# Kernel tuning notes

Hardware: AMD Instinct MI355X
Metric: run time of the kernel (lower is better)

The kernel has to match this reference:

```python
import jax, jax.numpy as jnp
import numpy as np


def setup_inputs() -> dict:
    key = jax.random.key(0)
    ks = jax.random.split(key, 10)
    B, HD, CD = 8192, 1024, 1024
    stdv = 1.0 / np.sqrt(HD)
    inp = {
        "hprev": jax.random.normal(ks[0], (B, HD), dtype=jnp.float32),
        "cprev": jax.random.normal(ks[1], (B, CD), dtype=jnp.float32),
        "w_hi": jax.random.uniform(ks[2], (HD, CD), jnp.float32, -stdv, stdv),
        "b_hi": jax.random.uniform(ks[3], (1, CD), jnp.float32, -stdv, stdv),
        "w_hf": jax.random.uniform(ks[4], (HD, CD), jnp.float32, -stdv, stdv),
        "b_hf": jax.random.uniform(ks[5], (1, CD), jnp.float32, -stdv, stdv),
        "w_hg": jax.random.uniform(ks[6], (HD, CD), jnp.float32, -stdv, stdv),
        "b_hg": jax.random.uniform(ks[7], (1, CD), jnp.float32, -stdv, stdv),
        "w_ho": jax.random.uniform(ks[8], (HD, CD), jnp.float32, -stdv, stdv),
        "b_ho": jax.random.uniform(ks[9], (1, CD), jnp.float32, -stdv, stdv),
    }
    return inp


def reference(hprev, cprev, w_hi, b_hi, w_hf, b_hf, w_hg, b_hg, w_ho, b_ho):
    # LSTM cell gates driven only by previous hidden state.
    i = jax.nn.sigmoid(hprev @ w_hi + b_hi)   # input gate  [B, CD]
    f = jax.nn.sigmoid(hprev @ w_hf + b_hf)   # forget gate [B, CD]
    g = jnp.tanh(hprev @ w_hg + b_hg)         # cell candidate
    o = jax.nn.sigmoid(hprev @ w_ho + b_ho)   # output gate
    cprime = f * cprev + i * g
    hprime = o * jnp.tanh(cprime)
    return (hprime, cprime)
```

## Files before the change

### kernel.cpp

```cpp
#include <hip/hip_runtime.h>
#include <hip/hip_bf16.h>
#include <stdint.h>

typedef short short8 __attribute__((ext_vector_type(8)));
typedef float f32x4 __attribute__((ext_vector_type(4)));
typedef unsigned short ushort4v __attribute__((ext_vector_type(4)));

#define MDIM 8192
#define KDIM 1024
#define NDIM 1024
#define NKT  16


__device__ __forceinline__ unsigned short f2bf(float f) {
  union { float f; unsigned int u; } v; v.f = f;
  unsigned int u = v.u;
  u += 0x7fffu + ((u >> 16) & 1u);
  return (unsigned short)(u >> 16);
}

__device__ __forceinline__ void load_lds16(const void* gsrc, void* ldst) {
  __builtin_amdgcn_global_load_lds(
      (__attribute__((address_space(1))) void*)gsrc,
      (__attribute__((address_space(3))) void*)ldst,
      16, 0, 0);
}

__device__ __forceinline__ float fast_sigmoid(float x) {
  return 1.0f / (1.0f + __expf(-x));
}

__device__ __forceinline__ float fast_tanh(float x) {
  x = fminf(30.0f, fmaxf(-30.0f, x));
  float e = __expf(-2.0f * x);
  return (1.0f - e) / (1.0f + e);
}


__global__ void convert_h_tiled(const float* __restrict__ in,
                                unsigned short* __restrict__ out, int nchunk) {
  int idx = blockIdx.x * blockDim.x + threadIdx.x;
  int stride = gridDim.x * blockDim.x;
  for (int i = idx; i < nchunk; i += stride) {
    int r = i >> 7;
    int kc8 = i & 127;
    const float4* src = reinterpret_cast<const float4*>(in + (size_t)r * KDIM + kc8 * 8);
    float4 v0 = src[0], v1 = src[1];
    short8 o;
    o[0] = (short)f2bf(v0.x); o[1] = (short)f2bf(v0.y);
    o[2] = (short)f2bf(v0.z); o[3] = (short)f2bf(v0.w);
    o[4] = (short)f2bf(v1.x); o[5] = (short)f2bf(v1.y);
    o[6] = (short)f2bf(v1.z); o[7] = (short)f2bf(v1.w);
    int kt = kc8 >> 3;
    int c8 = kc8 & 7;
    reinterpret_cast<short8*>(out)[((size_t)kt * MDIM + r) * 8 + c8] = o;
  }
}

__global__ void convert_w_tiled(const float* __restrict__ w0,
                                const float* __restrict__ w1,
                                const float* __restrict__ w2,
                                const float* __restrict__ w3,
                                unsigned short* __restrict__ out) {
  __shared__ float tile[64][65];
  int g = blockIdx.z;
  const float* w = (g == 0) ? w0 : (g == 1) ? w1 : (g == 2) ? w2 : w3;
  int kt = blockIdx.y;
  int k0 = kt * 64;
  int n0 = blockIdx.x * 64;
  int tx = threadIdx.x;
  int ty = threadIdx.y;
#pragma unroll
  for (int j = 0; j < 16; ++j) {
    int kk = ty * 16 + j;
    tile[kk][tx] = w[(size_t)(k0 + kk) * NDIM + n0 + tx];
  }
  __syncthreads();
#pragma unroll
  for (int j = 0; j < 16; ++j) {
    int nn = ty * 16 + j;
    out[(((size_t)kt * 4 + g) * NDIM + n0 + nn) * 64 + tx] = f2bf(tile[tx][nn]);
  }
}


#define BUF0 0
#define BUF1 65536

#define BARRIER() __builtin_amdgcn_s_barrier()
#define WAIT_LGKM0() do { \
    asm volatile("s_waitcnt lgkmcnt(0)" ::: "memory"); \
    __builtin_amdgcn_sched_barrier(0); } while (0)
#define WAIT_VM0() asm volatile("s_waitcnt vmcnt(0)" ::: "memory")

#define STAGE_A2(T, kA, j0) do { \
    load_lds16(ab + srcA + (kA) + (j0) * 8192,       lds + (T) + (j0) * 8192 + tid * 16); \
    load_lds16(ab + srcA + (kA) + ((j0) + 1) * 8192, lds + (T) + ((j0) + 1) * 8192 + tid * 16); } while (0)
#define STAGE_B2(T, kB, j0) do { \
    load_lds16(bb + srcB + (kB) + (j0) * 131072,       lds + (T) + 32768 + (j0) * 8192 + tid * 16); \
    load_lds16(bb + srcB + (kB) + ((j0) + 1) * 131072, lds + (T) + 32768 + ((j0) + 1) * 8192 + tid * 16); } while (0)

#define RD_A(S, m, s) (*(const short8*)(lds + (S) + a_base + (m) * 2048 + (s)))
#define RD_B(S, g, s) (*(const short8*)(lds + (S) + b_base + (g) * 8192 + (s)))

#define MFMA16(mb_) do { \
  _Pragma("unroll") \
  for (int mi = 0; mi < 4; ++mi) { \
    _Pragma("unroll") \
    for (int g = 0; g < 4; ++g) \
      acc[g][(mb_) + mi] = __builtin_amdgcn_mfma_f32_16x16x32_bf16( \
          Af[mi], Bf[g], acc[g][(mb_) + mi], 0, 0, 0); \
  } } while (0)

#define TILE(CUR, NXT, kA, kB) do { \
    short8 Af[4], Bf[4]; \
     \
    _Pragma("unroll") for (int g = 0; g < 4; ++g) Bf[g] = RD_B(CUR, g, s0); \
    _Pragma("unroll") for (int mi = 0; mi < 4; ++mi) Af[mi] = RD_A(CUR, mi, s0); \
    STAGE_A2(NXT, kA, 0); STAGE_A2(NXT, kA, 2); \
    BARRIER(); WAIT_LGKM0(); \
    __builtin_amdgcn_s_setprio(1); MFMA16(0); __builtin_amdgcn_s_setprio(0); \
    BARRIER(); \
     \
    _Pragma("unroll") for (int mi = 0; mi < 4; ++mi) Af[mi] = RD_A(CUR, 4 + mi, s0); \
    STAGE_B2(NXT, kB, 0); STAGE_B2(NXT, kB, 2); \
    BARRIER(); WAIT_LGKM0(); \
    __builtin_amdgcn_s_setprio(1); MFMA16(4); __builtin_amdgcn_s_setprio(0); \
    BARRIER(); \
     \
    _Pragma("unroll") for (int g = 0; g < 4; ++g) Bf[g] = RD_B(CUR, g, s1); \
    _Pragma("unroll") for (int mi = 0; mi < 4; ++mi) Af[mi] = RD_A(CUR, mi, s1); \
    BARRIER(); WAIT_LGKM0(); \
    __builtin_amdgcn_s_setprio(1); MFMA16(0); __builtin_amdgcn_s_setprio(0); \
    BARRIER(); \
     \
    _Pragma("unroll") for (int mi = 0; mi < 4; ++mi) Af[mi] = RD_A(CUR, 4 + mi, s1); \
    BARRIER(); WAIT_LGKM0(); \
    __builtin_amdgcn_s_setprio(1); MFMA16(4); __builtin_amdgcn_s_setprio(0); \
    WAIT_VM0(); \
    BARRIER(); } while (0)

__global__ __launch_bounds__(512, 2) void lstm_fused_gemm(
    const unsigned short* __restrict__ At,
    const unsigned short* __restrict__ Bt,
    const float* __restrict__ cprev,
    const float* __restrict__ b_i, const float* __restrict__ b_f,
    const float* __restrict__ b_g, const float* __restrict__ b_o,
    float* __restrict__ out)
{
  extern __shared__ unsigned char lds[];
  const int tid  = threadIdx.x;
  const int lane = tid & 63;
  const int wave = tid >> 6;
  const int wr = wave >> 2;
  const int wc = wave & 3;
  const int r15 = lane & 15;
  const int hh  = lane >> 4;

  int bid = blockIdx.x;
  int loc = bid >> 3;
  int mb = (bid & 7) * 4 + (loc >> 4);
  int nb = loc & 15;
  int brow = mb * 256;
  int bcol = nb * 64;

  const char* ab = (const char*)At;
  const char* bb = (const char*)Bt;

  const int rloc = tid >> 3;
  const int cx = (((tid & 7) ^ (rloc & 7)) << 4);
  const uint32_t srcA = (uint32_t)(brow + rloc) * 128 + cx;
  const uint32_t srcB = (uint32_t)(bcol + rloc) * 128 + cx;

  const int s0 = ((hh ^ (r15 & 7)) << 4);
  const int s1 = s0 ^ 64;
  const uint32_t a_base = (uint32_t)(wr * 128 + r15) * 128;
  const uint32_t b_base = 32768u + (uint32_t)(wc * 16 + r15) * 128;

  f32x4 acc[4][8];
#pragma unroll
  for (int g = 0; g < 4; ++g)
#pragma unroll
    for (int m = 0; m < 8; ++m)
      acc[g][m] = (f32x4){0.f, 0.f, 0.f, 0.f};

  STAGE_A2(BUF0, 0, 0); STAGE_A2(BUF0, 0, 2);
  STAGE_B2(BUF0, 0, 0); STAGE_B2(BUF0, 0, 2);
  WAIT_VM0();
  BARRIER();

  for (int it = 0; it < NKT / 2; ++it) {
    const uint32_t t1 = 2 * it + 1;
    const uint32_t t2 = (2 * it + 2) & (NKT - 1);
    {
      const uint32_t kA = t1 << 20, kB = t1 << 19;
      TILE(BUF0, BUF1, kA, kB);
    }
    {
      const uint32_t kA = t2 << 20, kB = t2 << 19;
      TILE(BUF1, BUF0, kA, kB);
    }
  }

  const size_t outC = (size_t)MDIM * NDIM;
  const int cc = bcol + wc * 16 + r15;
  const float bi = b_i[cc], bff = b_f[cc], bg = b_g[cc], bo = b_o[cc];
#pragma unroll
  for (int m = 0; m < 8; ++m) {
#pragma unroll
    for (int j = 0; j < 4; ++j) {
      int rr = brow + wr * 128 + m * 16 + hh * 4 + j;
      size_t base = (size_t)rr * NDIM + cc;
      float pi = acc[0][m][j] + bi;
      float pf = acc[1][m][j] + bff;
      float pg = acc[2][m][j] + bg;
      float po = acc[3][m][j] + bo;
      float iv = fast_sigmoid(pi);
      float fv = fast_sigmoid(pf);
      float gv = fast_tanh(pg);
      float ov = fast_sigmoid(po);
      float cp = fv * cprev[base] + iv * gv;
      float hp = ov * fast_tanh(cp);
      out[base] = hp;
      out[outC + base] = cp;
    }
  }
}


extern "C" void kernel_launch(void* const* d_in, const int* in_sizes, int n_in,
                              void* d_out, int out_size, void* d_ws, size_t ws_size,
                              hipStream_t stream) {
  const float* hprev = (const float*)d_in[0];
  const float* cprev = (const float*)d_in[1];
  const float* w_hi  = (const float*)d_in[2];
  const float* b_hi  = (const float*)d_in[3];
  const float* w_hf  = (const float*)d_in[4];
  const float* b_hf  = (const float*)d_in[5];
  const float* w_hg  = (const float*)d_in[6];
  const float* b_hg  = (const float*)d_in[7];
  const float* w_ho  = (const float*)d_in[8];
  const float* b_ho  = (const float*)d_in[9];
  float* out = (float*)d_out;

  unsigned short* At = (unsigned short*)d_ws;
  unsigned short* Bt = (unsigned short*)((char*)d_ws + (size_t)NKT * MDIM * 64 * 2);

  convert_h_tiled<<<2048, 256, 0, stream>>>(hprev, At, MDIM * KDIM / 8);
  convert_w_tiled<<<dim3(16, 16, 4), dim3(64, 4, 1), 0, stream>>>(
      w_hi, w_hf, w_hg, w_ho, Bt);
  lstm_fused_gemm<<<512, 512, 131072, stream>>>(At, Bt, cprev,
                                                b_hi, b_hf, b_hg, b_ho, out);
}
```

Before: 99.60 us.

## Load B fragments directly from global in MFMA-ready layout, halve LDS

The weight conversion now writes B in a fragment-linear layout, so each lane can load its MFMA B operand straight from global memory into registers, with one tile prefetched ahead. Only A is staged through LDS, which halves the shared memory to 64KB and removes most barriers and LDS waits in the inner loop. Block-to-tile mapping is also reordered so consecutive blocks share N columns. The trade-off is that B data is re-read from global/L2 by every block, and global load latency must be hidden by the register prefetch.

```diff
diff --git a/kernel.cpp b/kernel.cpp
--- a/kernel.cpp
+++ b/kernel.cpp
@@ -57,11 +57,11 @@
   }
 }
 
-__global__ void convert_w_tiled(const float* __restrict__ w0,
-                                const float* __restrict__ w1,
-                                const float* __restrict__ w2,
-                                const float* __restrict__ w3,
-                                unsigned short* __restrict__ out) {
+__global__ void convert_w_fraglin(const float* __restrict__ w0,
+                                  const float* __restrict__ w1,
+                                  const float* __restrict__ w2,
+                                  const float* __restrict__ w3,
+                                  unsigned short* __restrict__ out) {
   __shared__ float tile[64][65];
   int g = blockIdx.z;
   const float* w = (g == 0) ? w0 : (g == 1) ? w1 : (g == 2) ? w2 : w3;
@@ -77,78 +77,78 @@
   }
   __syncthreads();
 #pragma unroll
-  for (int j = 0; j < 16; ++j) {
-    int nn = ty * 16 + j;
-    out[(((size_t)kt * 4 + g) * NDIM + n0 + nn) * 64 + tx] = f2bf(tile[tx][nn]);
-  }
-}
-
-
-#define BUF0 0
-#define BUF1 65536
-
-#define BARRIER() __builtin_amdgcn_s_barrier()
-#define WAIT_LGKM0() do { \
-    asm volatile("s_waitcnt lgkmcnt(0)" ::: "memory"); \
-    __builtin_amdgcn_sched_barrier(0); } while (0)
-#define WAIT_VM0() asm volatile("s_waitcnt vmcnt(0)" ::: "memory")
-
-#define STAGE_A2(T, kA, j0) do { \
-    load_lds16(ab + srcA + (kA) + (j0) * 8192,       lds + (T) + (j0) * 8192 + tid * 16); \
-    load_lds16(ab + srcA + (kA) + ((j0) + 1) * 8192, lds + (T) + ((j0) + 1) * 8192 + tid * 16); } while (0)
-#define STAGE_B2(T, kB, j0) do { \
-    load_lds16(bb + srcB + (kB) + (j0) * 131072,       lds + (T) + 32768 + (j0) * 8192 + tid * 16); \
-    load_lds16(bb + srcB + (kB) + ((j0) + 1) * 131072, lds + (T) + 32768 + ((j0) + 1) * 8192 + tid * 16); } while (0)
-
-#define RD_A(S, m, s) (*(const short8*)(lds + (S) + a_base + (m) * 2048 + (s)))
-#define RD_B(S, g, s) (*(const short8*)(lds + (S) + b_base + (g) * 8192 + (s)))
-
-#define MFMA16(mb_) do { \
-  _Pragma("unroll") \
-  for (int mi = 0; mi < 4; ++mi) { \
+  for (int wit = 0; wit < 2; ++wit) {
+    int idx = ty * 2 + wit;
+    int kk = idx >> 2;
+    int sl = idx & 3;
+    short8 o;
+#pragma unroll
+    for (int e = 0; e < 8; ++e)
+      o[e] = (short)f2bf(tile[kk * 32 + (tx >> 4) * 8 + e][sl * 16 + (tx & 15)]);
+    reinterpret_cast<short8*>(out)[
+        ((((size_t)kt * 2 + kk) * 4 + g) * 64 + (n0 >> 4) + sl) * 64 + tx] = o;
+  }
+}
+
+
+#define BUFA0 0
+#define BUFA1 32768
+
+#define SB() __builtin_amdgcn_sched_barrier(0)
+
+#define LDA4(CUR, mb_, ss) do { \
+    Af0 = *(const short8*)(ldsb + (CUR) + ar + ((mb_) + 0) * 2048 + (ss)); \
+    Af1 = *(const short8*)(ldsb + (CUR) + ar + ((mb_) + 1) * 2048 + (ss)); \
+    Af2 = *(const short8*)(ldsb + (CUR) + ar + ((mb_) + 2) * 2048 + (ss)); \
+    Af3 = *(const short8*)(ldsb + (CUR) + ar + ((mb_) + 3) * 2048 + (ss)); } while (0)
+
+#define MROW(BP, m_, AF) do { \
+    acc[0][m_] = __builtin_amdgcn_mfma_f32_16x16x32_bf16(AF, BP##0, acc[0][m_], 0, 0, 0); \
+    acc[1][m_] = __builtin_amdgcn_mfma_f32_16x16x32_bf16(AF, BP##1, acc[1][m_], 0, 0, 0); \
+    acc[2][m_] = __builtin_amdgcn_mfma_f32_16x16x32_bf16(AF, BP##2, acc[2][m_], 0, 0, 0); \
+    acc[3][m_] = __builtin_amdgcn_mfma_f32_16x16x32_bf16(AF, BP##3, acc[3][m_], 0, 0, 0); } while (0)
+
+#define MFMA16(BP, mb_) do { \
+    __builtin_amdgcn_s_setprio(1); \
+    MROW(BP, (mb_) + 0, Af0); MROW(BP, (mb_) + 1, Af1); \
+    MROW(BP, (mb_) + 2, Af2); MROW(BP, (mb_) + 3, Af3); \
+    __builtin_amdgcn_s_setprio(0); } while (0)
+
+#define TILE(t_, CUR, NXT, BC, BN) do { \
+    const uint32_t tn_ = ((t_) + 1) & (NKT - 1); \
+    short8 q0, q1, q2, q3; \
+    SB(); \
+    q0 = *(const short8*)(bb + ((((uint32_t)(t_) * 2 + 1) * 4 + 0) << 16) + bv); \
+    q1 = *(const short8*)(bb + ((((uint32_t)(t_) * 2 + 1) * 4 + 1) << 16) + bv); \
+    q2 = *(const short8*)(bb + ((((uint32_t)(t_) * 2 + 1) * 4 + 2) << 16) + bv); \
+    q3 = *(const short8*)(bb + ((((uint32_t)(t_) * 2 + 1) * 4 + 3) << 16) + bv); \
+    SB(); \
     _Pragma("unroll") \
-    for (int g = 0; g < 4; ++g) \
-      acc[g][(mb_) + mi] = __builtin_amdgcn_mfma_f32_16x16x32_bf16( \
-          Af[mi], Bf[g], acc[g][(mb_) + mi], 0, 0, 0); \
-  } } while (0)
-
-#define TILE(CUR, NXT, kA, kB) do { \
-    short8 Af[4], Bf[4]; \
-     \
-    _Pragma("unroll") for (int g = 0; g < 4; ++g) Bf[g] = RD_B(CUR, g, s0); \
-    _Pragma("unroll") for (int mi = 0; mi < 4; ++mi) Af[mi] = RD_A(CUR, mi, s0); \
-    STAGE_A2(NXT, kA, 0); STAGE_A2(NXT, kA, 2); \
-    BARRIER(); WAIT_LGKM0(); \
-    __builtin_amdgcn_s_setprio(1); MFMA16(0); __builtin_amdgcn_s_setprio(0); \
-    BARRIER(); \
-     \
-    _Pragma("unroll") for (int mi = 0; mi < 4; ++mi) Af[mi] = RD_A(CUR, 4 + mi, s0); \
-    STAGE_B2(NXT, kB, 0); STAGE_B2(NXT, kB, 2); \
-    BARRIER(); WAIT_LGKM0(); \
-    __builtin_amdgcn_s_setprio(1); MFMA16(4); __builtin_amdgcn_s_setprio(0); \
-    BARRIER(); \
-     \
-    _Pragma("unroll") for (int g = 0; g < 4; ++g) Bf[g] = RD_B(CUR, g, s1); \
-    _Pragma("unroll") for (int mi = 0; mi < 4; ++mi) Af[mi] = RD_A(CUR, mi, s1); \
-    BARRIER(); WAIT_LGKM0(); \
-    __builtin_amdgcn_s_setprio(1); MFMA16(0); __builtin_amdgcn_s_setprio(0); \
-    BARRIER(); \
-     \
-    _Pragma("unroll") for (int mi = 0; mi < 4; ++mi) Af[mi] = RD_A(CUR, 4 + mi, s1); \
-    BARRIER(); WAIT_LGKM0(); \
-    __builtin_amdgcn_s_setprio(1); MFMA16(4); __builtin_amdgcn_s_setprio(0); \
-    WAIT_VM0(); \
-    BARRIER(); } while (0)
+    for (int j = 0; j < 4; ++j) \
+      load_lds16(ab + ((size_t)tn_ << 20) + srcA + j * 8192, \
+                 ldsb + (NXT) + j * 8192 + tid * 16); \
+    SB(); \
+    BN##0 = *(const short8*)(bb + (((tn_ * 2 + 0) * 4 + 0) << 16) + bv); \
+    BN##1 = *(const short8*)(bb + (((tn_ * 2 + 0) * 4 + 1) << 16) + bv); \
+    BN##2 = *(const short8*)(bb + (((tn_ * 2 + 0) * 4 + 2) << 16) + bv); \
+    BN##3 = *(const short8*)(bb + (((tn_ * 2 + 0) * 4 + 3) << 16) + bv); \
+    SB(); \
+    LDA4(CUR, 0, s0v); MFMA16(BC, 0); \
+    LDA4(CUR, 4, s0v); MFMA16(BC, 4); \
+    LDA4(CUR, 0, s1v); MFMA16(q, 0); \
+    LDA4(CUR, 4, s1v); MFMA16(q, 4); \
+    asm volatile("s_waitcnt vmcnt(4)" ::: "memory"); \
+    __builtin_amdgcn_s_barrier(); } while (0)
 
 __global__ __launch_bounds__(512, 2) void lstm_fused_gemm(
     const unsigned short* __restrict__ At,
-    const unsigned short* __restrict__ Bt,
+    const unsigned short* __restrict__ Blin,
     const float* __restrict__ cprev,
     const float* __restrict__ b_i, const float* __restrict__ b_f,
     const float* __restrict__ b_g, const float* __restrict__ b_o,
     float* __restrict__ out)
 {
-  extern __shared__ unsigned char lds[];
+  __shared__ unsigned char ldsb[65536];
   const int tid  = threadIdx.x;
   const int lane = tid & 63;
   const int wave = tid >> 6;
@@ -159,23 +159,23 @@
 
   int bid = blockIdx.x;
   int loc = bid >> 3;
-  int mb = (bid & 7) * 4 + (loc >> 4);
-  int nb = loc & 15;
+  int nb = (bid & 7) * 2 + (loc >> 5);
+  int mb = loc & 31;
   int brow = mb * 256;
   int bcol = nb * 64;
 
   const char* ab = (const char*)At;
-  const char* bb = (const char*)Bt;
-
-  const int rloc = tid >> 3;
-  const int cx = (((tid & 7) ^ (rloc & 7)) << 4);
-  const uint32_t srcA = (uint32_t)(brow + rloc) * 128 + cx;
-  const uint32_t srcB = (uint32_t)(bcol + rloc) * 128 + cx;
-
-  const int s0 = ((hh ^ (r15 & 7)) << 4);
-  const int s1 = s0 ^ 64;
-  const uint32_t a_base = (uint32_t)(wr * 128 + r15) * 128;
-  const uint32_t b_base = 32768u + (uint32_t)(wc * 16 + r15) * 128;
+  const char* bb = (const char*)Blin;
+
+  const int arow = tid >> 3;
+  const int cx = (((tid & 7) ^ (arow & 7)) << 4);
+  const uint32_t srcA = (uint32_t)(brow + arow) * 128 + cx;
+
+  const uint32_t ar = (uint32_t)(wr * 128 + r15) * 128;
+  const int s0v = ((hh ^ (r15 & 7)) << 4);
+  const int s1v = s0v ^ 64;
+
+  const uint32_t bv = ((uint32_t)(nb * 4 + wc) << 10) + lane * 16;
 
   f32x4 acc[4][8];
 #pragma unroll
@@ -184,22 +184,22 @@
     for (int m = 0; m < 8; ++m)
       acc[g][m] = (f32x4){0.f, 0.f, 0.f, 0.f};
 
-  STAGE_A2(BUF0, 0, 0); STAGE_A2(BUF0, 0, 2);
-  STAGE_B2(BUF0, 0, 0); STAGE_B2(BUF0, 0, 2);
-  WAIT_VM0();
-  BARRIER();
+  short8 Af0, Af1, Af2, Af3;
+  short8 bA0, bA1, bA2, bA3, bB0, bB1, bB2, bB3;
+
+#pragma unroll
+  for (int j = 0; j < 4; ++j)
+    load_lds16(ab + srcA + j * 8192, ldsb + BUFA0 + j * 8192 + tid * 16);
+  bA0 = *(const short8*)(bb + (0u << 16) + bv);
+  bA1 = *(const short8*)(bb + (1u << 16) + bv);
+  bA2 = *(const short8*)(bb + (2u << 16) + bv);
+  bA3 = *(const short8*)(bb + (3u << 16) + bv);
+  asm volatile("s_waitcnt vmcnt(0)" ::: "memory");
+  __builtin_amdgcn_s_barrier();
 
   for (int it = 0; it < NKT / 2; ++it) {
-    const uint32_t t1 = 2 * it + 1;
-    const uint32_t t2 = (2 * it + 2) & (NKT - 1);
-    {
-      const uint32_t kA = t1 << 20, kB = t1 << 19;
-      TILE(BUF0, BUF1, kA, kB);
-    }
-    {
-      const uint32_t kA = t2 << 20, kB = t2 << 19;
-      TILE(BUF1, BUF0, kA, kB);
-    }
+    TILE(2 * it,     BUFA0, BUFA1, bA, bB);
+    TILE(2 * it + 1, BUFA1, BUFA0, bB, bA);
   }
 
   const size_t outC = (size_t)MDIM * NDIM;
@@ -243,12 +243,12 @@
   const float* b_ho  = (const float*)d_in[9];
   float* out = (float*)d_out;
 
-  unsigned short* At = (unsigned short*)d_ws;
-  unsigned short* Bt = (unsigned short*)((char*)d_ws + (size_t)NKT * MDIM * 64 * 2);
+  unsigned short* At   = (unsigned short*)d_ws;
+  unsigned short* Blin = (unsigned short*)((char*)d_ws + (size_t)NKT * MDIM * 64 * 2);
 
   convert_h_tiled<<<2048, 256, 0, stream>>>(hprev, At, MDIM * KDIM / 8);
-  convert_w_tiled<<<dim3(16, 16, 4), dim3(64, 4, 1), 0, stream>>>(
-      w_hi, w_hf, w_hg, w_ho, Bt);
-  lstm_fused_gemm<<<512, 512, 131072, stream>>>(At, Bt, cprev,
-                                                b_hi, b_hf, b_hg, b_ho, out);
-}
+  convert_w_fraglin<<<dim3(16, 16, 4), dim3(64, 4, 1), 0, stream>>>(
+      w_hi, w_hf, w_hg, w_ho, Blin);
+  lstm_fused_gemm<<<512, 512, 0, stream>>>(At, Blin, cprev,
+                                           b_hi, b_hf, b_hg, b_ho, out);
+}
```

After: 110.0 us. +10.4%, slower.

## Restructure GEMM main loop into quadrant-wise MFMA with deeper partial-wait prefetch

Applied to the files above, without the earlier changes.

Reworks the K-loop so each wave loads all B fragments for both K-halves at once and computes in 2x2 quadrants of (M,N), reusing registers across both K sub-steps. Staging is reordered so the next tiles' A/B loads are issued into the buffer being freed mid-tile, using vmcnt(6) partial waits instead of draining all loads each tile. The block-to-tile mapping is also changed to group by N-column. This aims to overlap global->LDS traffic with MFMAs more deeply and cut LDS reads, at the cost of more registers and tricky buffer-hazard ordering.

```diff
diff --git a/kernel.cpp b/kernel.cpp
--- a/kernel.cpp
+++ b/kernel.cpp
@@ -4,7 +4,6 @@
 
 typedef short short8 __attribute__((ext_vector_type(8)));
 typedef float f32x4 __attribute__((ext_vector_type(4)));
-typedef unsigned short ushort4v __attribute__((ext_vector_type(4)));
 
 #define MDIM 8192
 #define KDIM 1024
@@ -84,61 +83,58 @@
 }
 
 
-#define BUF0 0
-#define BUF1 65536
-
-#define BARRIER() __builtin_amdgcn_s_barrier()
-#define WAIT_LGKM0() do { \
+#define X0 0
+#define X1 65536
+
+#define BAR() __builtin_amdgcn_s_barrier()
+#define LGKM0() do { \
     asm volatile("s_waitcnt lgkmcnt(0)" ::: "memory"); \
     __builtin_amdgcn_sched_barrier(0); } while (0)
-#define WAIT_VM0() asm volatile("s_waitcnt vmcnt(0)" ::: "memory")
-
-#define STAGE_A2(T, kA, j0) do { \
-    load_lds16(ab + srcA + (kA) + (j0) * 8192,       lds + (T) + (j0) * 8192 + tid * 16); \
-    load_lds16(ab + srcA + (kA) + ((j0) + 1) * 8192, lds + (T) + ((j0) + 1) * 8192 + tid * 16); } while (0)
-#define STAGE_B2(T, kB, j0) do { \
-    load_lds16(bb + srcB + (kB) + (j0) * 131072,       lds + (T) + 32768 + (j0) * 8192 + tid * 16); \
-    load_lds16(bb + srcB + (kB) + ((j0) + 1) * 131072, lds + (T) + 32768 + ((j0) + 1) * 8192 + tid * 16); } while (0)
-
-#define RD_A(S, m, s) (*(const short8*)(lds + (S) + a_base + (m) * 2048 + (s)))
-#define RD_B(S, g, s) (*(const short8*)(lds + (S) + b_base + (g) * 8192 + (s)))
-
-#define MFMA16(mb_) do { \
-  _Pragma("unroll") \
-  for (int mi = 0; mi < 4; ++mi) { \
-    _Pragma("unroll") \
-    for (int g = 0; g < 4; ++g) \
-      acc[g][(mb_) + mi] = __builtin_amdgcn_mfma_f32_16x16x32_bf16( \
-          Af[mi], Bf[g], acc[g][(mb_) + mi], 0, 0, 0); \
-  } } while (0)
-
-#define TILE(CUR, NXT, kA, kB) do { \
-    short8 Af[4], Bf[4]; \
-     \
-    _Pragma("unroll") for (int g = 0; g < 4; ++g) Bf[g] = RD_B(CUR, g, s0); \
-    _Pragma("unroll") for (int mi = 0; mi < 4; ++mi) Af[mi] = RD_A(CUR, mi, s0); \
-    STAGE_A2(NXT, kA, 0); STAGE_A2(NXT, kA, 2); \
-    BARRIER(); WAIT_LGKM0(); \
-    __builtin_amdgcn_s_setprio(1); MFMA16(0); __builtin_amdgcn_s_setprio(0); \
-    BARRIER(); \
-     \
-    _Pragma("unroll") for (int mi = 0; mi < 4; ++mi) Af[mi] = RD_A(CUR, 4 + mi, s0); \
-    STAGE_B2(NXT, kB, 0); STAGE_B2(NXT, kB, 2); \
-    BARRIER(); WAIT_LGKM0(); \
-    __builtin_amdgcn_s_setprio(1); MFMA16(4); __builtin_amdgcn_s_setprio(0); \
-    BARRIER(); \
-     \
-    _Pragma("unroll") for (int g = 0; g < 4; ++g) Bf[g] = RD_B(CUR, g, s1); \
-    _Pragma("unroll") for (int mi = 0; mi < 4; ++mi) Af[mi] = RD_A(CUR, mi, s1); \
-    BARRIER(); WAIT_LGKM0(); \
-    __builtin_amdgcn_s_setprio(1); MFMA16(0); __builtin_amdgcn_s_setprio(0); \
-    BARRIER(); \
-     \
-    _Pragma("unroll") for (int mi = 0; mi < 4; ++mi) Af[mi] = RD_A(CUR, 4 + mi, s1); \
-    BARRIER(); WAIT_LGKM0(); \
-    __builtin_amdgcn_s_setprio(1); MFMA16(4); __builtin_amdgcn_s_setprio(0); \
-    WAIT_VM0(); \
-    BARRIER(); } while (0)
+#define VM6() asm volatile("s_waitcnt vmcnt(6)" ::: "memory")
+
+#define STG_A(BUF, ktv, h) do { \
+    const uint32_t _oA = ((uint32_t)(ktv) << 20) + srcA + (h) * 16384; \
+    load_lds16(ab + _oA,        ldsb + (BUF) + (h) * 16384 + tid * 16); \
+    load_lds16(ab + _oA + 8192, ldsb + (BUF) + (h) * 16384 + 8192 + tid * 16); } while (0)
+#define STG_B(BUF, ktv, h) do { \
+    const uint32_t _oB = ((uint32_t)(ktv) << 19) + srcB0 + (h) * 262144; \
+    load_lds16(bb + _oB,          ldsb + (BUF) + 32768 + (h) * 16384 + tid * 16); \
+    load_lds16(bb + _oB + 131072, ldsb + (BUF) + 32768 + (h) * 16384 + 8192 + tid * 16); } while (0)
+
+#define LDB_ALL(CB) do { \
+    _Pragma("unroll") for (int g = 0; g < 4; ++g) { \
+      Br[g * 2 + 0] = *(const short8*)(ldsb + (CB) + b_base + g * 8192 + s0v); \
+      Br[g * 2 + 1] = *(const short8*)(ldsb + (CB) + b_base + g * 8192 + s1v); } } while (0)
+#define LDA_Q(CB, qm) do { \
+    _Pragma("unroll") for (int f = 0; f < 4; ++f) { \
+      Ar[f * 2 + 0] = *(const short8*)(ldsb + (CB) + a_base + ((qm) * 64 + f * 16) * 128 + s0v); \
+      Ar[f * 2 + 1] = *(const short8*)(ldsb + (CB) + a_base + ((qm) * 64 + f * 16) * 128 + s1v); } } while (0)
+
+#define MFMAQ(qm, qn) do { \
+    __builtin_amdgcn_s_setprio(1); \
+    _Pragma("unroll") for (int kk = 0; kk < 2; ++kk) \
+    _Pragma("unroll") for (int f = 0; f < 4; ++f) \
+    _Pragma("unroll") for (int gg = 0; gg < 2; ++gg) \
+      acc[(qn) * 2 + gg][(qm) * 4 + f] = __builtin_amdgcn_mfma_f32_16x16x32_bf16( \
+          Ar[f * 2 + kk], Br[((qn) * 2 + gg) * 2 + kk], \
+          acc[(qn) * 2 + gg][(qm) * 4 + f], 0, 0, 0); \
+    __builtin_amdgcn_s_setprio(0); } while (0)
+
+#define BLOCK4(CB, OB, tA1, tN2) do { \
+     \
+    LDB_ALL(CB); LDA_Q(CB, 0); \
+    STG_A(OB, tA1, 1); \
+    BAR(); LGKM0(); MFMAQ(0, 0); BAR(); \
+     \
+    STG_B(CB, tN2, 0); \
+    BAR(); MFMAQ(0, 1); BAR(); \
+     \
+    LDA_Q(CB, 1); \
+    STG_B(CB, tN2, 1); \
+    BAR(); LGKM0(); MFMAQ(1, 0); BAR(); \
+     \
+    STG_A(CB, tN2, 0); \
+    BAR(); MFMAQ(1, 1); VM6(); BAR(); } while (0)
 
 __global__ __launch_bounds__(512, 2) void lstm_fused_gemm(
     const unsigned short* __restrict__ At,
@@ -148,7 +144,7 @@
     const float* __restrict__ b_g, const float* __restrict__ b_o,
     float* __restrict__ out)
 {
-  extern __shared__ unsigned char lds[];
+  extern __shared__ unsigned char ldsb[];
   const int tid  = threadIdx.x;
   const int lane = tid & 63;
   const int wave = tid >> 6;
@@ -159,23 +155,23 @@
 
   int bid = blockIdx.x;
   int loc = bid >> 3;
-  int mb = (bid & 7) * 4 + (loc >> 4);
-  int nb = loc & 15;
+  int nb = (bid & 7) * 2 + (loc >> 5);
+  int mb = loc & 31;
   int brow = mb * 256;
   int bcol = nb * 64;
 
   const char* ab = (const char*)At;
   const char* bb = (const char*)Bt;
 
-  const int rloc = tid >> 3;
-  const int cx = (((tid & 7) ^ (rloc & 7)) << 4);
-  const uint32_t srcA = (uint32_t)(brow + rloc) * 128 + cx;
-  const uint32_t srcB = (uint32_t)(bcol + rloc) * 128 + cx;
-
-  const int s0 = ((hh ^ (r15 & 7)) << 4);
-  const int s1 = s0 ^ 64;
+  const int srow = tid >> 3;
+  const int cx = (((tid & 7) ^ (srow & 7)) << 4);
+  const uint32_t srcA  = (uint32_t)(brow + srow) * 128 + cx;
+  const uint32_t srcB0 = (uint32_t)(bcol + srow) * 128 + cx;
+
   const uint32_t a_base = (uint32_t)(wr * 128 + r15) * 128;
   const uint32_t b_base = 32768u + (uint32_t)(wc * 16 + r15) * 128;
+  const int s0v = ((hh ^ (r15 & 7)) << 4);
+  const int s1v = s0v ^ 64;
 
   f32x4 acc[4][8];
 #pragma unroll
@@ -184,22 +180,19 @@
     for (int m = 0; m < 8; ++m)
       acc[g][m] = (f32x4){0.f, 0.f, 0.f, 0.f};
 
-  STAGE_A2(BUF0, 0, 0); STAGE_A2(BUF0, 0, 2);
-  STAGE_B2(BUF0, 0, 0); STAGE_B2(BUF0, 0, 2);
-  WAIT_VM0();
-  BARRIER();
+  short8 Ar[8], Br[8];
+
+  STG_A(X0, 0, 0); STG_A(X0, 0, 1);
+  STG_B(X0, 0, 0); STG_B(X0, 0, 1);
+  STG_B(X1, 1, 0); STG_B(X1, 1, 1);
+  STG_A(X1, 1, 0);
+  VM6();
+  BAR();
 
   for (int it = 0; it < NKT / 2; ++it) {
-    const uint32_t t1 = 2 * it + 1;
-    const uint32_t t2 = (2 * it + 2) & (NKT - 1);
-    {
-      const uint32_t kA = t1 << 20, kB = t1 << 19;
-      TILE(BUF0, BUF1, kA, kB);
-    }
-    {
-      const uint32_t kA = t2 << 20, kB = t2 << 19;
-      TILE(BUF1, BUF0, kA, kB);
-    }
+    const int t0 = 2 * it;
+    BLOCK4(X0, X1, (t0 + 1) & 15, (t0 + 2) & 15);
+    BLOCK4(X1, X0, (t0 + 2) & 15, (t0 + 3) & 15);
   }
 
   const size_t outC = (size_t)MDIM * NDIM;
```

Result: slower. 105.6 us (+6.1%).
